# Kernel optimization log

Measured on AMD Instinct MI355X. Metric: run time of the kernel, lower is better.

Reference implementation:

```python
import jax, jax.numpy as jnp
import numpy as np

B, S, D, H = 2, 2048, 1024, 16
DK = D // H  # 64
ROPE_BASE = 10000.0


def _rope_tables(dk, seq_len, base=ROPE_BASE):
    inv_freq = 1.0 / base ** (jnp.arange(0, dk, 2, dtype=jnp.float32) / dk)
    t = jnp.arange(seq_len, dtype=jnp.float32)
    freqs = t[:, None] * inv_freq[None, :]            # [S, dk/2]
    cos = jnp.repeat(jnp.cos(freqs), 2, axis=-1)      # [S, dk] (repeat_interleave)
    sin = jnp.repeat(jnp.sin(freqs), 2, axis=-1)
    return cos, sin


def _rotate_half(x):
    x1, x2 = jnp.split(x, 2, axis=-1)
    return jnp.concatenate((-x2, x1), axis=-1)


def setup_inputs() -> dict:
    key = jax.random.key(0)
    ks = jax.random.split(key, 9)
    scale = 0.02
    x = jax.random.normal(ks[0], (B, S, D), jnp.float32)
    wq = jax.random.normal(ks[1], (D, D), jnp.float32) * scale
    wk = jax.random.normal(ks[2], (D, D), jnp.float32) * scale
    wv = jax.random.normal(ks[3], (D, D), jnp.float32) * scale
    wo = jax.random.normal(ks[4], (D, D), jnp.float32) * scale
    bq = jnp.zeros((D,), jnp.float32)
    bk = jnp.zeros((D,), jnp.float32)
    bv = jnp.zeros((D,), jnp.float32)
    bo = jnp.zeros((D,), jnp.float32)
    mask = jnp.tril(jnp.ones((S, S), dtype=bool))[None, None]  # [1,1,S,S] causal
    return {"x": x, "mask": mask, "wq": wq, "bq": bq, "wk": wk, "bk": bk,
            "wv": wv, "bv": bv, "wo": wo, "bo": bo}


def reference(x, mask, wq, bq, wk, bk, wv, bv, wo, bo):
    b, s, d = x.shape
    h, dk = H, DK
    # QKV projections (nn.Linear: x @ W^T + b), split heads -> [B,H,S,dk]
    q = (x @ wq.T + bq).reshape(b, s, h, dk).transpose(0, 2, 1, 3)
    k = (x @ wk.T + bk).reshape(b, s, h, dk).transpose(0, 2, 1, 3)
    v = (x @ wv.T + bv).reshape(b, s, h, dk).transpose(0, 2, 1, 3)
    # RoPE
    cos, sin = _rope_tables(dk, s)                    # [S, dk]
    cos = cos[None, None]                             # [1,1,S,dk]
    sin = sin[None, None]
    q = q * cos + _rotate_half(q) * sin
    k = k * cos + _rotate_half(k) * sin
    # Naive attention: full [B,H,S,S] scores
    scores = jnp.einsum("bhqd,bhkd->bhqk", q, k) / np.float32(np.sqrt(dk))
    scores = jnp.where(mask, scores, jnp.float32(-1e9))
    attn = jax.nn.softmax(scores, axis=-1)
    out = jnp.einsum("bhqk,bhkd->bhqd", attn, v)      # [B,H,S,dk]
    out = out.transpose(0, 2, 1, 3).reshape(b, s, d)  # [B,S,D]
    return out @ wo.T + bo
```

## Files before the change

### kernel.cpp

```cpp
#include <hip/hip_runtime.h>
#include <hip/hip_bf16.h>

#define B_ 2
#define S_ 2048
#define D_ 1024
#define H_ 16
#define DK_ 64
#define BH_ (B_*H_)

typedef __attribute__((ext_vector_type(8))) short short8;
typedef __attribute__((ext_vector_type(4))) short short4v;
typedef __attribute__((ext_vector_type(4))) float f32x4;

__device__ __forceinline__ unsigned short f2bf(float f) {
  unsigned u = __float_as_uint(f);
  u += 0x7FFFu + ((u >> 16) & 1u);
  return (unsigned short)(u >> 16);
}
__device__ __forceinline__ float bf2f(unsigned short b) {
  return __uint_as_float(((unsigned)b) << 16);
}
__device__ __forceinline__ unsigned pk2bf(float lo, float hi) {
  float2 f; f.x = lo; f.y = hi;
  __hip_bfloat162 t = __float22bfloat162_rn(f);
  unsigned r; __builtin_memcpy(&r, &t, 4); return r;
}

__device__ __forceinline__ long ftile_off(int n, int k, int ktiles) {
  return ((long)(n >> 7) * ktiles + (k >> 5)) * 4096 + ((k >> 3) & 3) * 1024 + (n & 127) * 8 + (k & 7);
}

__global__ void cvt_kernel(const float* __restrict__ x, const float* __restrict__ wq,
                           const float* __restrict__ wk, const float* __restrict__ wv,
                           const float* __restrict__ wo, const float* __restrict__ bq,
                           const float* __restrict__ bk, const float* __restrict__ bv,
                           unsigned short* __restrict__ xb, unsigned short* __restrict__ wqkvb,
                           unsigned short* __restrict__ wob, float* __restrict__ bqkv) {
  long idx = ((long)blockIdx.x * blockDim.x + threadIdx.x) * 4;
  const long NX = (long)B_ * S_ * D_;
  const long NW = (long)D_ * D_;
  if (idx < NX) {
    float4 v = *(const float4*)(x + idx);
    short4v o; o[0] = f2bf(v.x); o[1] = f2bf(v.y); o[2] = f2bf(v.z); o[3] = f2bf(v.w);
    const int m = (int)(idx >> 10), k = (int)(idx & 1023);
    *(short4v*)(xb + ftile_off(m, k, 32)) = o;
    return;
  }
  idx -= NX;
  if (idx < 3 * NW) {
    const float* w = (idx < NW) ? wq : ((idx < 2 * NW) ? wk : wv);
    float4 v = *(const float4*)(w + (idx & (NW - 1)));
    short4v o; o[0] = f2bf(v.x); o[1] = f2bf(v.y); o[2] = f2bf(v.z); o[3] = f2bf(v.w);
    const int n = (int)(idx >> 10), k = (int)(idx & 1023);
    *(short4v*)(wqkvb + ftile_off(n, k, 32)) = o;
    return;
  }
  idx -= 3 * NW;
  if (idx < NW) {
    float4 v = *(const float4*)(wo + idx);
    short4v o; o[0] = f2bf(v.x); o[1] = f2bf(v.y); o[2] = f2bf(v.z); o[3] = f2bf(v.w);
    const int n = (int)(idx >> 10), k = (int)(idx & 1023);
    *(short4v*)(wob + ftile_off(n, k, 32)) = o;
    return;
  }
  idx -= NW;
  if (idx < 3 * D_) {
    const float* bb = (idx < D_) ? (bq + idx) : ((idx < 2 * D_) ? (bk + idx - D_) : (bv + idx - 2 * D_));
    *(float4*)(bqkv + idx) = *(const float4*)bb;
  }
}

template<bool OUT_F32>
__global__ __launch_bounds__(256) void gemm_bt(const unsigned short* __restrict__ A,
                                               const unsigned short* __restrict__ Bm,
                                               const float* __restrict__ bias,
                                               void* __restrict__ Cp, int M, int N, int K) {
  __shared__ alignas(16) unsigned short As[4096];
  __shared__ alignas(16) unsigned short Bs[4096];
  const int t = threadIdx.x;
  const int w = t >> 6;
  const int lane = t & 63;
  const int brow = blockIdx.y * 128;
  const int bcol = blockIdx.x * 128;
  const int wr = (w >> 1) * 64, wc = (w & 1) * 64;
  const int fr = lane & 15;
  const int g = lane >> 4;
  const int ktiles = K >> 5;
  f32x4 acc[4][4] = {};

  for (int kt = 0; kt < ktiles; ++kt) {
    const unsigned short* Asrc = A  + ((long)blockIdx.y * ktiles + kt) * 4096;
    const unsigned short* Bsrc = Bm + ((long)blockIdx.x * ktiles + kt) * 4096;
#pragma unroll
    for (int j = 0; j < 2; ++j) {
      const int off = (w * 2 + j) * 512;
      __builtin_amdgcn_global_load_lds((const __attribute__((address_space(1))) void*)(Asrc + off + lane * 8),
                                       (__attribute__((address_space(3))) void*)(As + off), 16, 0, 0);
      __builtin_amdgcn_global_load_lds((const __attribute__((address_space(1))) void*)(Bsrc + off + lane * 8),
                                       (__attribute__((address_space(3))) void*)(Bs + off), 16, 0, 0);
    }
    __syncthreads();
    short8 a[4], b[4];
#pragma unroll
    for (int m = 0; m < 4; ++m)
      a[m] = *(const short8*)(As + g * 1024 + (wr + m * 16 + fr) * 8);
#pragma unroll
    for (int n = 0; n < 4; ++n)
      b[n] = *(const short8*)(Bs + g * 1024 + (wc + n * 16 + fr) * 8);
#pragma unroll
    for (int m = 0; m < 4; ++m)
#pragma unroll
      for (int n = 0; n < 4; ++n)
        acc[m][n] = __builtin_amdgcn_mfma_f32_16x16x32_bf16(a[m], b[n], acc[m][n], 0, 0, 0);
    __syncthreads();
  }

  const int fg = g;
#pragma unroll
  for (int m = 0; m < 4; ++m) {
#pragma unroll
    for (int n = 0; n < 4; ++n) {
      const int col = bcol + wc + n * 16 + fr;
      const float bv_ = bias[col];
#pragma unroll
      for (int i = 0; i < 4; ++i) {
        const int row = brow + wr + m * 16 + fg * 4 + i;
        const float v = acc[m][n][i] + bv_;
        if (OUT_F32) ((float*)Cp)[(long)row * N + col] = v;
        else ((unsigned short*)Cp)[(long)row * N + col] = f2bf(v);
      }
    }
  }
}

__global__ void rope_kernel(const unsigned short* __restrict__ qkv,
                            unsigned short* __restrict__ Qh,
                            unsigned short* __restrict__ Kf) {
  const int idx = blockIdx.x * blockDim.x + threadIdx.x;
  const int d = idx & 63;
  const int s = (idx >> 6) & (S_ - 1);
  const int bh = idx >> 17;
  const int b = bh >> 4, h = bh & 15;
  const long qrow = (long)(b * S_ + s) * 3072 + h * 64;
  const float qv = bf2f(qkv[qrow + d]);
  const float kv = bf2f(qkv[qrow + 1024 + d]);
  const int dp = (d < 32) ? d + 32 : d - 32;
  const float qp = bf2f(qkv[qrow + dp]);
  const float kp = bf2f(qkv[qrow + 1024 + dp]);
  const int j = d >> 1;
  const float invf = __expf(-(float)j * 0.28782313662425574f);
  const float fr = (float)s * invf;
  float sn, cs;
  __sincosf(fr, &sn, &cs);
  const float qo = (d < 32) ? (qv * cs - qp * sn) : (qv * cs + qp * sn);
  const float ko = (d < 32) ? (kv * cs - kp * sn) : (kv * cs + kp * sn);
  Qh[(long)bh * S_ * DK_ + (long)s * DK_ + d] = f2bf(qo * 0.125f);
  const long kfo = (long)bh * (S_ * DK_) + (long)(s >> 4) * 1024 +
                   (long)(d >> 5) * 512 + (long)((d >> 3) & 3) * 128 + (s & 15) * 8 + (d & 7);
  Kf[kfo] = f2bf(ko);
}

__global__ __launch_bounds__(256) void vtrans_kernel(const unsigned short* __restrict__ qkv,
                                                     unsigned short* __restrict__ Vf) {
  __shared__ unsigned short tile[32][72];
  const int bh = blockIdx.y;
  const int b = bh >> 4, h = bh & 15;
  const int c32 = blockIdx.x;
  const int tid = threadIdx.x;
  {
    const int r = tid >> 3, d0 = (tid & 7) * 8;
    *(short8*)&tile[r][d0] =
        *(const short8*)(qkv + (long)(b * S_ + c32 * 32 + r) * 3072 + 2048 + h * 64 + d0);
  }
  __syncthreads();
  const int t = tid >> 6, g = (tid >> 4) & 3, fr = tid & 15;
  short8 o;
#pragma unroll
  for (int j = 0; j < 8; ++j) {
    const int r = (j < 4) ? (4 * g + j) : (16 + 4 * g + (j - 4));
    o[j] = tile[r][t * 16 + fr];
  }
  *(short8*)(Vf + ((long)(bh * 64 + c32)) * 2048 + t * 512 + g * 128 + fr * 8) = o;
}

__global__ __launch_bounds__(256) void flash_kernel(const unsigned short* __restrict__ Qh,
                                                    const unsigned short* __restrict__ Kf,
                                                    const unsigned short* __restrict__ Vf,
                                                    unsigned short* __restrict__ attnout) {
  __shared__ alignas(16) unsigned short Ks[4096];
  __shared__ alignas(16) unsigned short Vs[4096];

  const int flat = (int)blockIdx.x;
  const int xcd = flat & 7;
  const int ix  = flat >> 3;
  const int k   = ix >> 5;
  const int c   = ix & 31;
  const int bh  = xcd * 4 + k;
  const int qblk = (k & 1) ? c : 31 - c;

  const int b = bh >> 4, h = bh & 15;
  const int w = threadIdx.x >> 6, lane = threadIdx.x & 63;
  const int fr = lane & 15, g = lane >> 4;
  const int qg = qblk * 64 + w * 16 + fr;

  const unsigned short* Qb = Qh + (long)bh * (S_ * DK_);
  const short8 qf0 = *(const short8*)(Qb + (long)qg * DK_ + g * 8);
  const short8 qf1 = *(const short8*)(Qb + (long)qg * DK_ + 32 + g * 8);

  short8 vone;
#pragma unroll
  for (int i = 0; i < 8; ++i) vone[i] = (short)0x3F80;

  f32x4 acc[4] = {};
  f32x4 acl = {};

  const unsigned short* kfb = Kf + (long)bh * (S_ * DK_);
  const unsigned short* vfb = Vf + (long)bh * (S_ * DK_);
  const int kvend = qblk * 64;
  const int frag = g * 128 + fr * 8;

  for (int kv0 = 0; kv0 <= kvend; kv0 += 64) {
    {
      const unsigned short* gk = kfb + (long)kv0 * 64 + w * 1024 + lane * 8;
      unsigned short* lk = Ks + w * 1024;
      __builtin_amdgcn_global_load_lds((const __attribute__((address_space(1))) void*)gk,
                                       (__attribute__((address_space(3))) void*)lk, 16, 0, 0);
      __builtin_amdgcn_global_load_lds((const __attribute__((address_space(1))) void*)(gk + 512),
                                       (__attribute__((address_space(3))) void*)(lk + 512), 16, 0, 0);
      const unsigned short* gv = vfb + (long)kv0 * 64 + w * 1024 + lane * 8;
      unsigned short* lv = Vs + w * 1024;
      __builtin_amdgcn_global_load_lds((const __attribute__((address_space(1))) void*)gv,
                                       (__attribute__((address_space(3))) void*)lv, 16, 0, 0);
      __builtin_amdgcn_global_load_lds((const __attribute__((address_space(1))) void*)(gv + 512),
                                       (__attribute__((address_space(3))) void*)(lv + 512), 16, 0, 0);
    }
    __syncthreads();

    f32x4 st[4];
    __builtin_amdgcn_s_setprio(1);
#pragma unroll
    for (int cc = 0; cc < 4; ++cc) {
      const short8 k0 = *(const short8*)(Ks + cc * 1024 + frag);
      const short8 k1 = *(const short8*)(Ks + cc * 1024 + 512 + frag);
      f32x4 z = {};
      z = __builtin_amdgcn_mfma_f32_16x16x32_bf16(k0, qf0, z, 0, 0, 0);
      z = __builtin_amdgcn_mfma_f32_16x16x32_bf16(k1, qf1, z, 0, 0, 0);
      st[cc] = z;
    }
    __builtin_amdgcn_s_setprio(0);

    float sv[16];
#pragma unroll
    for (int cc = 0; cc < 4; ++cc)
#pragma unroll
      for (int i = 0; i < 4; ++i) sv[cc * 4 + i] = st[cc][i];

    if (kv0 == kvend) {
#pragma unroll
      for (int cc = 0; cc < 4; ++cc)
#pragma unroll
        for (int i = 0; i < 4; ++i)
          if (cc * 16 + g * 4 + i > w * 16 + fr) sv[cc * 4 + i] = -3.0e38f;
    }

    float ps[16];
#pragma unroll
    for (int i = 0; i < 16; ++i) ps[i] = __expf(sv[i]);

    union { short8 s8; unsigned u[4]; } P0, P1;
#pragma unroll
    for (int i = 0; i < 4; ++i) {
      P0.u[i] = pk2bf(ps[2 * i], ps[2 * i + 1]);
      P1.u[i] = pk2bf(ps[8 + 2 * i], ps[8 + 2 * i + 1]);
    }

    __builtin_amdgcn_s_setprio(1);
#pragma unroll
    for (int t = 0; t < 4; ++t) {
      const short8 va = *(const short8*)(Vs + t * 512 + frag);
      const short8 vb = *(const short8*)(Vs + 2048 + t * 512 + frag);
      acc[t] = __builtin_amdgcn_mfma_f32_16x16x32_bf16(va, P0.s8, acc[t], 0, 0, 0);
      acc[t] = __builtin_amdgcn_mfma_f32_16x16x32_bf16(vb, P1.s8, acc[t], 0, 0, 0);
    }
    acl = __builtin_amdgcn_mfma_f32_16x16x32_bf16(vone, P0.s8, acl, 0, 0, 0);
    acl = __builtin_amdgcn_mfma_f32_16x16x32_bf16(vone, P1.s8, acl, 0, 0, 0);
    __builtin_amdgcn_s_setprio(0);
    __syncthreads();
  }

  const float ri = 1.0f / acl[0];
  const int row = b * S_ + qg;
#pragma unroll
  for (int t = 0; t < 4; ++t) {
    short4v ov;
#pragma unroll
    for (int i = 0; i < 4; ++i) ov[i] = (short)f2bf(acc[t][i] * ri);
    const int kcol = h * 64 + t * 16 + g * 4;
    *(short4v*)(attnout + ftile_off(row, kcol, 32)) = ov;
  }
}

extern "C" void kernel_launch(void* const* d_in, const int* in_sizes, int n_in,
                              void* d_out, int out_size, void* d_ws, size_t ws_size,
                              hipStream_t stream) {
  const float* x  = (const float*)d_in[0];
  const float* wq = (const float*)d_in[2];
  const float* bq = (const float*)d_in[3];
  const float* wk = (const float*)d_in[4];
  const float* bk = (const float*)d_in[5];
  const float* wv = (const float*)d_in[6];
  const float* bv = (const float*)d_in[7];
  const float* wo = (const float*)d_in[8];
  const float* bo = (const float*)d_in[9];

  const long NX = (long)B_ * S_ * D_;
  const long NW = (long)D_ * D_;

  unsigned short* xb    = (unsigned short*)d_ws;
  unsigned short* wqkvb = xb + NX;
  unsigned short* wob   = wqkvb + 3 * NW;
  float*          bqkv  = (float*)(wob + NW);
  unsigned short* qkv   = (unsigned short*)(bqkv + 3 * D_);
  unsigned short* Qh    = qkv + (long)(B_ * S_) * 3 * D_;
  unsigned short* Kf    = Qh + NX;
  unsigned short* Vf    = Kf + NX;
  unsigned short* attnout = xb;

  const long ncvt4 = (NX + 3 * NW + NW + 3 * D_) / 4;
  cvt_kernel<<<(int)((ncvt4 + 255) / 256), 256, 0, stream>>>(x, wq, wk, wv, wo, bq, bk, bv,
                                                             xb, wqkvb, wob, bqkv);
  gemm_bt<false><<<dim3(24, 32), 256, 0, stream>>>(xb, wqkvb, bqkv, qkv, 4096, 3072, 1024);
  rope_kernel<<<(int)(NX / 256), 256, 0, stream>>>(qkv, Qh, Kf);
  vtrans_kernel<<<dim3(64, BH_), 256, 0, stream>>>(qkv, Vf);
  flash_kernel<<<1024, 256, 0, stream>>>(Qh, Kf, Vf, attnout);
  gemm_bt<true><<<dim3(8, 32), 256, 0, stream>>>(attnout, wob, bo, d_out, 4096, 1024, 1024);
}
```

Baseline: 133.5 us.

## Stage cvt output through LDS, widen flash KV tile, use exp2

The fp32-to-bf16 conversion kernel now converts one 128x32 tile per block, stages it in LDS and writes it out as contiguous 16-byte chunks instead of scattered 8-byte stores. The flash kernel loads 128 KV rows per barrier, processed as two 64-row sub-steps, which halves the number of syncthreads and load phases. Softmax now uses the raw v_exp_f32 (exp2) instruction, with log2(e) folded into the Q scale. The larger KV tile doubles LDS use per block, which may lower occupancy, and the masked step now covers up to 128 rows.

Result: faster. 122.1 us (-8.5%).

```diff
diff --git a/kernel.cpp b/kernel.cpp
--- a/kernel.cpp
+++ b/kernel.cpp
@@ -25,49 +25,57 @@
   __hip_bfloat162 t = __float22bfloat162_rn(f);
   unsigned r; __builtin_memcpy(&r, &t, 4); return r;
 }
+__device__ __forceinline__ float fexp2(float x) {
+  float r; asm("v_exp_f32 %0, %1" : "=v"(r) : "v"(x)); return r;
+}
 
 __device__ __forceinline__ long ftile_off(int n, int k, int ktiles) {
   return ((long)(n >> 7) * ktiles + (k >> 5)) * 4096 + ((k >> 3) & 3) * 1024 + (n & 127) * 8 + (k & 7);
 }
 
-__global__ void cvt_kernel(const float* __restrict__ x, const float* __restrict__ wq,
+__global__ __launch_bounds__(256) void cvt_kernel(const float* __restrict__ x, const float* __restrict__ wq,
                            const float* __restrict__ wk, const float* __restrict__ wv,
                            const float* __restrict__ wo, const float* __restrict__ bq,
                            const float* __restrict__ bk, const float* __restrict__ bv,
                            unsigned short* __restrict__ xb, unsigned short* __restrict__ wqkvb,
                            unsigned short* __restrict__ wob, float* __restrict__ bqkv) {
-  long idx = ((long)blockIdx.x * blockDim.x + threadIdx.x) * 4;
-  const long NX = (long)B_ * S_ * D_;
-  const long NW = (long)D_ * D_;
-  if (idx < NX) {
-    float4 v = *(const float4*)(x + idx);
-    short4v o; o[0] = f2bf(v.x); o[1] = f2bf(v.y); o[2] = f2bf(v.z); o[3] = f2bf(v.w);
-    const int m = (int)(idx >> 10), k = (int)(idx & 1023);
-    *(short4v*)(xb + ftile_off(m, k, 32)) = o;
+  const int bi = blockIdx.x;
+  if (bi >= 2048) {
+    const int i = (bi - 2048) * 1024 + (int)threadIdx.x * 4;
+    const float* bb = (i < D_) ? (bq + i) : ((i < 2 * D_) ? (bk + i - D_) : (bv + i - 2 * D_));
+    *(float4*)(bqkv + i) = *(const float4*)bb;
     return;
   }
-  idx -= NX;
-  if (idx < 3 * NW) {
-    const float* w = (idx < NW) ? wq : ((idx < 2 * NW) ? wk : wv);
-    float4 v = *(const float4*)(w + (idx & (NW - 1)));
-    short4v o; o[0] = f2bf(v.x); o[1] = f2bf(v.y); o[2] = f2bf(v.z); o[3] = f2bf(v.w);
-    const int n = (int)(idx >> 10), k = (int)(idx & 1023);
-    *(short4v*)(wqkvb + ftile_off(n, k, 32)) = o;
-    return;
-  }
-  idx -= 3 * NW;
-  if (idx < NW) {
-    float4 v = *(const float4*)(wo + idx);
-    short4v o; o[0] = f2bf(v.x); o[1] = f2bf(v.y); o[2] = f2bf(v.z); o[3] = f2bf(v.w);
-    const int n = (int)(idx >> 10), k = (int)(idx & 1023);
-    *(short4v*)(wob + ftile_off(n, k, 32)) = o;
-    return;
-  }
-  idx -= NW;
-  if (idx < 3 * D_) {
-    const float* bb = (idx < D_) ? (bq + idx) : ((idx < 2 * D_) ? (bk + idx - D_) : (bv + idx - 2 * D_));
-    *(float4*)(bqkv + idx) = *(const float4*)bb;
-  }
+  __shared__ alignas(16) unsigned short lt[4096];
+  const int t = threadIdx.x;
+  const int r = t >> 1, kb = (t & 1) * 16;
+  int ti; unsigned short* dst;
+  if (bi < 1024) { ti = bi; dst = xb; }
+  else if (bi < 1792) { ti = bi - 1024; dst = wqkvb; }
+  else { ti = bi - 1792; dst = wob; }
+  const int rt = ti >> 5, kt = ti & 31;
+  const int grow = rt * 128 + r;
+  const float* sp;
+  if (bi < 1024) sp = x + (long)grow * 1024 + kt * 32 + kb;
+  else if (bi < 1792) {
+    const float* w = (grow < 1024) ? wq : ((grow < 2048) ? wk : wv);
+    sp = w + (long)(grow & 1023) * 1024 + kt * 32 + kb;
+  } else sp = wo + (long)grow * 1024 + kt * 32 + kb;
+
+  const float4 va = ((const float4*)sp)[0], vb = ((const float4*)sp)[1];
+  const float4 vc = ((const float4*)sp)[2], vd = ((const float4*)sp)[3];
+  short8 o0, o1;
+  o0[0] = f2bf(va.x); o0[1] = f2bf(va.y); o0[2] = f2bf(va.z); o0[3] = f2bf(va.w);
+  o0[4] = f2bf(vb.x); o0[5] = f2bf(vb.y); o0[6] = f2bf(vb.z); o0[7] = f2bf(vb.w);
+  o1[0] = f2bf(vc.x); o1[1] = f2bf(vc.y); o1[2] = f2bf(vc.z); o1[3] = f2bf(vc.w);
+  o1[4] = f2bf(vd.x); o1[5] = f2bf(vd.y); o1[6] = f2bf(vd.z); o1[7] = f2bf(vd.w);
+  const int kc0 = kb >> 3;
+  *(short8*)(lt + kc0 * 1024 + r * 8) = o0;
+  *(short8*)(lt + (kc0 + 1) * 1024 + r * 8) = o1;
+  __syncthreads();
+  unsigned short* dp = dst + ((long)rt * 32 + kt) * 4096 + t * 16;
+  *(short8*)dp       = *(const short8*)(lt + t * 16);
+  *(short8*)(dp + 8) = *(const short8*)(lt + t * 16 + 8);
 }
 
 template<bool OUT_F32>
@@ -115,7 +123,6 @@
     __syncthreads();
   }
 
-  const int fg = g;
 #pragma unroll
   for (int m = 0; m < 4; ++m) {
 #pragma unroll
@@ -124,7 +131,7 @@
       const float bv_ = bias[col];
 #pragma unroll
       for (int i = 0; i < 4; ++i) {
-        const int row = brow + wr + m * 16 + fg * 4 + i;
+        const int row = brow + wr + m * 16 + g * 4 + i;
         const float v = acc[m][n][i] + bv_;
         if (OUT_F32) ((float*)Cp)[(long)row * N + col] = v;
         else ((unsigned short*)Cp)[(long)row * N + col] = f2bf(v);
@@ -154,7 +161,7 @@
   __sincosf(fr, &sn, &cs);
   const float qo = (d < 32) ? (qv * cs - qp * sn) : (qv * cs + qp * sn);
   const float ko = (d < 32) ? (kv * cs - kp * sn) : (kv * cs + kp * sn);
-  Qh[(long)bh * S_ * DK_ + (long)s * DK_ + d] = f2bf(qo * 0.125f);
+  Qh[(long)bh * S_ * DK_ + (long)s * DK_ + d] = f2bf(qo * 0.18033688011112043f);
   const long kfo = (long)bh * (S_ * DK_) + (long)(s >> 4) * 1024 +
                    (long)(d >> 5) * 512 + (long)((d >> 3) & 3) * 128 + (s & 15) * 8 + (d & 7);
   Kf[kfo] = f2bf(ko);
@@ -187,8 +194,8 @@
                                                     const unsigned short* __restrict__ Kf,
                                                     const unsigned short* __restrict__ Vf,
                                                     unsigned short* __restrict__ attnout) {
-  __shared__ alignas(16) unsigned short Ks[4096];
-  __shared__ alignas(16) unsigned short Vs[4096];
+  __shared__ alignas(16) unsigned short Ks[8192];
+  __shared__ alignas(16) unsigned short Vs[8192];
 
   const int flat = (int)blockIdx.x;
   const int xcd = flat & 7;
@@ -219,72 +226,75 @@
   const int kvend = qblk * 64;
   const int frag = g * 128 + fr * 8;
 
-  for (int kv0 = 0; kv0 <= kvend; kv0 += 64) {
+  for (int kv0 = 0; kv0 <= kvend; kv0 += 128) {
     {
-      const unsigned short* gk = kfb + (long)kv0 * 64 + w * 1024 + lane * 8;
-      unsigned short* lk = Ks + w * 1024;
-      __builtin_amdgcn_global_load_lds((const __attribute__((address_space(1))) void*)gk,
-                                       (__attribute__((address_space(3))) void*)lk, 16, 0, 0);
-      __builtin_amdgcn_global_load_lds((const __attribute__((address_space(1))) void*)(gk + 512),
-                                       (__attribute__((address_space(3))) void*)(lk + 512), 16, 0, 0);
-      const unsigned short* gv = vfb + (long)kv0 * 64 + w * 1024 + lane * 8;
-      unsigned short* lv = Vs + w * 1024;
-      __builtin_amdgcn_global_load_lds((const __attribute__((address_space(1))) void*)gv,
-                                       (__attribute__((address_space(3))) void*)lv, 16, 0, 0);
-      __builtin_amdgcn_global_load_lds((const __attribute__((address_space(1))) void*)(gv + 512),
-                                       (__attribute__((address_space(3))) void*)(lv + 512), 16, 0, 0);
+      const unsigned short* gk = kfb + (long)kv0 * 64 + w * 2048 + lane * 8;
+      unsigned short* lk = Ks + w * 2048;
+      const unsigned short* gv = vfb + (long)kv0 * 64 + w * 2048 + lane * 8;
+      unsigned short* lv = Vs + w * 2048;
+#pragma unroll
+      for (int cc = 0; cc < 4; ++cc) {
+        __builtin_amdgcn_global_load_lds((const __attribute__((address_space(1))) void*)(gk + cc * 512),
+                                         (__attribute__((address_space(3))) void*)(lk + cc * 512), 16, 0, 0);
+        __builtin_amdgcn_global_load_lds((const __attribute__((address_space(1))) void*)(gv + cc * 512),
+                                         (__attribute__((address_space(3))) void*)(lv + cc * 512), 16, 0, 0);
+      }
     }
     __syncthreads();
-
-    f32x4 st[4];
-    __builtin_amdgcn_s_setprio(1);
-#pragma unroll
-    for (int cc = 0; cc < 4; ++cc) {
-      const short8 k0 = *(const short8*)(Ks + cc * 1024 + frag);
-      const short8 k1 = *(const short8*)(Ks + cc * 1024 + 512 + frag);
-      f32x4 z = {};
-      z = __builtin_amdgcn_mfma_f32_16x16x32_bf16(k0, qf0, z, 0, 0, 0);
-      z = __builtin_amdgcn_mfma_f32_16x16x32_bf16(k1, qf1, z, 0, 0, 0);
-      st[cc] = z;
+    const bool domask = (kv0 + 128 > kvend);
+
+#pragma unroll
+    for (int sub = 0; sub < 2; ++sub) {
+      const unsigned short* ksb = Ks + sub * 4096;
+      const unsigned short* vsb = Vs + sub * 4096;
+
+      f32x4 st[4];
+      __builtin_amdgcn_s_setprio(1);
+#pragma unroll
+      for (int cc = 0; cc < 4; ++cc) {
+        const short8 k0 = *(const short8*)(ksb + cc * 1024 + frag);
+        const short8 k1 = *(const short8*)(ksb + cc * 1024 + 512 + frag);
+        f32x4 z = {};
+        z = __builtin_amdgcn_mfma_f32_16x16x32_bf16(k0, qf0, z, 0, 0, 0);
+        z = __builtin_amdgcn_mfma_f32_16x16x32_bf16(k1, qf1, z, 0, 0, 0);
+        st[cc] = z;
+      }
+      __builtin_amdgcn_s_setprio(0);
+
+      if (domask) {
+        const int base = kv0 + sub * 64 + g * 4;
+#pragma unroll
+        for (int cc = 0; cc < 4; ++cc)
+#pragma unroll
+          for (int i = 0; i < 4; ++i)
+            if (base + cc * 16 + i > qg) st[cc][i] = -3.0e38f;
+      }
+
+      float ps[16];
+#pragma unroll
+      for (int cc = 0; cc < 4; ++cc)
+#pragma unroll
+        for (int i = 0; i < 4; ++i) ps[cc * 4 + i] = fexp2(st[cc][i]);
+
+      union { short8 s8; unsigned u[4]; } P0, P1;
+#pragma unroll
+      for (int i = 0; i < 4; ++i) {
+        P0.u[i] = pk2bf(ps[2 * i], ps[2 * i + 1]);
+        P1.u[i] = pk2bf(ps[8 + 2 * i], ps[8 + 2 * i + 1]);
+      }
+
+      __builtin_amdgcn_s_setprio(1);
+#pragma unroll
+      for (int t = 0; t < 4; ++t) {
+        const short8 va = *(const short8*)(vsb + t * 512 + frag);
+        const short8 vb = *(const short8*)(vsb + 2048 + t * 512 + frag);
+        acc[t] = __builtin_amdgcn_mfma_f32_16x16x32_bf16(va, P0.s8, acc[t], 0, 0, 0);
+        acc[t] = __builtin_amdgcn_mfma_f32_16x16x32_bf16(vb, P1.s8, acc[t], 0, 0, 0);
+      }
+      acl = __builtin_amdgcn_mfma_f32_16x16x32_bf16(vone, P0.s8, acl, 0, 0, 0);
+      acl = __builtin_amdgcn_mfma_f32_16x16x32_bf16(vone, P1.s8, acl, 0, 0, 0);
+      __builtin_amdgcn_s_setprio(0);
     }
-    __builtin_amdgcn_s_setprio(0);
-
-    float sv[16];
-#pragma unroll
-    for (int cc = 0; cc < 4; ++cc)
-#pragma unroll
-      for (int i = 0; i < 4; ++i) sv[cc * 4 + i] = st[cc][i];
-
-    if (kv0 == kvend) {
-#pragma unroll
-      for (int cc = 0; cc < 4; ++cc)
-#pragma unroll
-        for (int i = 0; i < 4; ++i)
-          if (cc * 16 + g * 4 + i > w * 16 + fr) sv[cc * 4 + i] = -3.0e38f;
-    }
-
-    float ps[16];
-#pragma unroll
-    for (int i = 0; i < 16; ++i) ps[i] = __expf(sv[i]);
-
-    union { short8 s8; unsigned u[4]; } P0, P1;
-#pragma unroll
-    for (int i = 0; i < 4; ++i) {
-      P0.u[i] = pk2bf(ps[2 * i], ps[2 * i + 1]);
-      P1.u[i] = pk2bf(ps[8 + 2 * i], ps[8 + 2 * i + 1]);
-    }
-
-    __builtin_amdgcn_s_setprio(1);
-#pragma unroll
-    for (int t = 0; t < 4; ++t) {
-      const short8 va = *(const short8*)(Vs + t * 512 + frag);
-      const short8 vb = *(const short8*)(Vs + 2048 + t * 512 + frag);
-      acc[t] = __builtin_amdgcn_mfma_f32_16x16x32_bf16(va, P0.s8, acc[t], 0, 0, 0);
-      acc[t] = __builtin_amdgcn_mfma_f32_16x16x32_bf16(vb, P1.s8, acc[t], 0, 0, 0);
-    }
-    acl = __builtin_amdgcn_mfma_f32_16x16x32_bf16(vone, P0.s8, acl, 0, 0, 0);
-    acl = __builtin_amdgcn_mfma_f32_16x16x32_bf16(vone, P1.s8, acl, 0, 0, 0);
-    __builtin_amdgcn_s_setprio(0);
     __syncthreads();
   }
 
@@ -326,9 +336,8 @@
   unsigned short* Vf    = Kf + NX;
   unsigned short* attnout = xb;
 
-  const long ncvt4 = (NX + 3 * NW + NW + 3 * D_) / 4;
-  cvt_kernel<<<(int)((ncvt4 + 255) / 256), 256, 0, stream>>>(x, wq, wk, wv, wo, bq, bk, bv,
-                                                             xb, wqkvb, wob, bqkv);
+  cvt_kernel<<<2051, 256, 0, stream>>>(x, wq, wk, wv, wo, bq, bk, bv,
+                                       xb, wqkvb, wob, bqkv);
   gemm_bt<false><<<dim3(24, 32), 256, 0, stream>>>(xb, wqkvb, bqkv, qkv, 4096, 3072, 1024);
   rope_kernel<<<(int)(NX / 256), 256, 0, stream>>>(qkv, Qh, Kf);
   vtrans_kernel<<<dim3(64, BH_), 256, 0, stream>>>(qkv, Vf);
```
